# Kernel tuning notes

Hardware: AMD Instinct MI355X
Metric: run time of the kernel (lower is better)

## Reference

```python
import jax, jax.numpy as jnp
import numpy as np
import math

HIDDEN = 384
HEADS = 4
HEAD_DIM = HIDDEN // HEADS
B, T = 8, 2048


def _shift_rel(pos_tensor):
    # pos_tensor: [b, h, t, 2t-1] -> [b, h, t, t] (Transformer-XL shift trick)
    b, h, t, n = pos_tensor.shape
    zero_pad = jnp.zeros((b, h, t, 1), dtype=pos_tensor.dtype)
    padded = jnp.concatenate([zero_pad, pos_tensor], axis=-1)  # [b,h,t,n+1]
    padded = padded.reshape(b, h, n + 1, t)
    shifted = padded[:, :, 1:].reshape(b, h, t, n)
    return shifted[:, :, :, : n // 2 + 1]  # [b,h,t,t]


def setup_inputs() -> dict:
    key = jax.random.key(0)
    ks = jax.random.split(key, 12)
    s = 1.0 / math.sqrt(HIDDEN)
    inp = {
        "hidden_states": jax.random.normal(ks[0], (B, T, HIDDEN), jnp.float32),
        "pos_emb": jax.random.normal(ks[1], (1, 2 * T - 1, HIDDEN), jnp.float32),
        "attention_mask": jnp.ones((B, 1, T), jnp.int32),
        "Wq": jax.random.normal(ks[2], (HIDDEN, HIDDEN), jnp.float32) * s,
        "bq": jnp.zeros((HIDDEN,), jnp.float32),
        "Wk": jax.random.normal(ks[3], (HIDDEN, HIDDEN), jnp.float32) * s,
        "bk": jnp.zeros((HIDDEN,), jnp.float32),
        "Wv": jax.random.normal(ks[4], (HIDDEN, HIDDEN), jnp.float32) * s,
        "bv": jnp.zeros((HIDDEN,), jnp.float32),
        "Wo": jax.random.normal(ks[5], (HIDDEN, HIDDEN), jnp.float32) * s,
        "bo": jnp.zeros((HIDDEN,), jnp.float32),
        "Wpos": jax.random.normal(ks[6], (HIDDEN, HIDDEN), jnp.float32) * s,
        "pos_bias_u": jax.random.normal(ks[7], (HEADS, HEAD_DIM), jnp.float32) * s,
        "pos_bias_v": jax.random.normal(ks[8], (HEADS, HEAD_DIM), jnp.float32) * s,
    }
    return inp


def reference(hidden_states, pos_emb, attention_mask, Wq, bq, Wk, bk, Wv, bv,
              Wo, bo, Wpos, pos_bias_u, pos_bias_v):
    bsz, q_len, _ = hidden_states.shape
    # projections (nn.Linear applies x @ W.T + b; weights here stored as [in, out])
    q = (hidden_states @ Wq + bq).reshape(bsz, q_len, HEADS, HEAD_DIM)
    k = (hidden_states @ Wk + bk).reshape(bsz, q_len, HEADS, HEAD_DIM)
    v = (hidden_states @ Wv + bv).reshape(bsz, q_len, HEADS, HEAD_DIM)
    pos = (pos_emb @ Wpos).reshape(pos_emb.shape[0], -1, HEADS, HEAD_DIM)

    q_u = (q + pos_bias_u).transpose(0, 2, 1, 3)  # [b,h,t,d]
    q_v = (q + pos_bias_v).transpose(0, 2, 1, 3)

    # content score: [b,h,t,t]
    matrix_ac = jnp.einsum('bhqd,bkhd->bhqk', q_u, k)
    # position score: [b,h,t,2t-1] then shift
    matrix_bd = jnp.einsum('bhqd,pnhd->bhqn', q_v, pos)
    matrix_bd = _shift_rel(matrix_bd)

    scores = (matrix_ac + matrix_bd) / math.sqrt(HEAD_DIM)

    mask = (attention_mask[:, None] == 0)  # [b,1,1,t]
    min_val = jnp.finfo(scores.dtype).min
    scores = jnp.where(mask, min_val, scores)
    attn = jax.nn.softmax(scores, axis=-1)
    attn = jnp.where(mask, 0.0, attn)

    out = jnp.einsum('bhqk,bkhd->bqhd', attn, v).reshape(bsz, q_len, HIDDEN)
    return out @ Wo + bo
```

## Files before the change

### kernel.cpp

```cpp
#include <hip/hip_runtime.h>
#include <hip/hip_bf16.h>

#define TSEQ 2048
#define HID 384
#define NHEAD 4
#define HD 96
#define NBATCH 8

using bf16 = __bf16;
typedef bf16 bf16x8 __attribute__((ext_vector_type(8)));
typedef bf16 bf16x4 __attribute__((ext_vector_type(4)));
typedef float f32x4 __attribute__((ext_vector_type(4)));

static __device__ __forceinline__ f32x4 mfma16(bf16x8 a, bf16x8 b, f32x4 c) {
    return __builtin_amdgcn_mfma_f32_16x16x32_bf16(a, b, c, 0, 0, 0);
}

__global__ void k_conv8(const float* __restrict__ src, bf16* __restrict__ dst, int n8) {
    int t = blockIdx.x * 256 + threadIdx.x;
    if (t >= n8) return;
    const float4* s4 = reinterpret_cast<const float4*>(src);
    float4 a = s4[2 * t], b = s4[2 * t + 1];
    bf16x8 o;
    o[0] = (bf16)a.x; o[1] = (bf16)a.y; o[2] = (bf16)a.z; o[3] = (bf16)a.w;
    o[4] = (bf16)b.x; o[5] = (bf16)b.y; o[6] = (bf16)b.z; o[7] = (bf16)b.w;
    *reinterpret_cast<bf16x8*>(dst + 8 * t) = o;
}

__global__ void k_convT(const float* __restrict__ W, bf16* __restrict__ WT) {
    int t = blockIdx.x * 256 + threadIdx.x;
    int n = t / HID, k = t % HID;
    WT[t] = (bf16)W[(size_t)k * HID + n];
}

__launch_bounds__(256, 2)
__global__ void k_proj(const bf16* __restrict__ X, const bf16* __restrict__ P,
                       const bf16* __restrict__ wqT, const bf16* __restrict__ wkT,
                       const bf16* __restrict__ wvT, const bf16* __restrict__ wpT,
                       const float* __restrict__ bq, const float* __restrict__ bk,
                       const float* __restrict__ bv,
                       const float* __restrict__ pbu, const float* __restrict__ pbv,
                       bf16* __restrict__ qu, bf16* __restrict__ qv,
                       bf16* __restrict__ kws, bf16* __restrict__ vt,
                       bf16* __restrict__ pp) {
    __shared__ bf16 wt_lds[96][392];
    const float SC = 0.10206207262f;
    int mat = blockIdx.z;
    int m0 = blockIdx.x * 64;
    if (mat == 3 && m0 >= 4095) return;
    int n0 = blockIdx.y * 96;
    const bf16* A  = (mat == 3) ? P : X;
    const bf16* WT = (mat == 0) ? wqT : (mat == 1) ? wkT : (mat == 2) ? wvT : wpT;
    int tid = threadIdx.x;
    #pragma unroll
    for (int s = 0; s < 18; ++s) {
        int cc = tid + 256 * s;
        int r = cc / 48, ch = cc % 48;
        *reinterpret_cast<int4*>(&wt_lds[r][ch * 8]) =
            *reinterpret_cast<const int4*>(WT + (size_t)(n0 + r) * HID + ch * 8);
    }
    __syncthreads();
    int lane = tid & 63, w = tid >> 6;
    int c = lane & 15, g = lane >> 4;
    int arow = m0 + 16 * w + c;
    if (mat == 3 && arow > 4095) arow = 4095;
    const bf16* Abase = A + (size_t)arow * HID + 8 * g;
    f32x4 acc[6] = {};
    for (int ks = 0; ks < 12; ++ks) {
        bf16x8 a = *reinterpret_cast<const bf16x8*>(Abase + 32 * ks);
        #pragma unroll
        for (int jt = 0; jt < 6; ++jt) {
            bf16x8 b = *reinterpret_cast<const bf16x8*>(&wt_lds[16 * jt + c][32 * ks + 8 * g]);
            acc[jt] = mfma16(a, b, acc[jt]);
        }
    }
    int h = blockIdx.y;
    int rbase = m0 + 16 * w + 4 * g;
    if (mat == 0) {
        #pragma unroll
        for (int jt = 0; jt < 6; ++jt) {
            int n = n0 + 16 * jt + c;
            int d = 16 * jt + c;
            float bb = bq[n], bu = pbu[n], bvv = pbv[n];
            #pragma unroll
            for (int j = 0; j < 4; ++j) {
                int m = rbase + j;
                int b_ = m >> 11, t = m & 2047;
                size_t o = (((size_t)(b_ * NHEAD + h)) * TSEQ + t) * HD + d;
                float q = acc[jt][j] + bb;
                qu[o] = (bf16)((q + bu) * SC);
                qv[o] = (bf16)((q + bvv) * SC);
            }
        }
    } else if (mat == 1) {
        #pragma unroll
        for (int jt = 0; jt < 6; ++jt) {
            int n = n0 + 16 * jt + c;
            int d = 16 * jt + c;
            float bb = bk[n];
            #pragma unroll
            for (int j = 0; j < 4; ++j) {
                int m = rbase + j;
                int b_ = m >> 11, t = m & 2047;
                size_t o = (((size_t)(b_ * NHEAD + h)) * TSEQ + t) * HD + d;
                kws[o] = (bf16)(acc[jt][j] + bb);
            }
        }
    } else if (mat == 2) {
        #pragma unroll
        for (int jt = 0; jt < 6; ++jt) {
            int d = 16 * jt + c;
            float bb = bv[n0 + 16 * jt + c];
            int m = rbase;
            int b_ = m >> 11, t0 = m & 2047;
            size_t o = (((size_t)(b_ * NHEAD + h)) * HD + d) * TSEQ + t0;
            bf16x4 pk;
            #pragma unroll
            for (int j = 0; j < 4; ++j) pk[j] = (bf16)(acc[jt][j] + bb);
            *reinterpret_cast<bf16x4*>(vt + o) = pk;
        }
    } else {
        #pragma unroll
        for (int jt = 0; jt < 6; ++jt) {
            int d = 16 * jt + c;
            #pragma unroll
            for (int j = 0; j < 4; ++j) {
                int m = rbase + j;
                if (m < 4095) {
                    size_t o = ((size_t)h * 4096 + m) * HD + d;
                    pp[o] = (bf16)acc[jt][j];
                }
            }
        }
    }
}

__launch_bounds__(256, 2)
__global__ void k_attn(const bf16* __restrict__ qu, const bf16* __restrict__ qv,
                       const bf16* __restrict__ kws, const bf16* __restrict__ vt,
                       const bf16* __restrict__ pp, const int* __restrict__ mask,
                       bf16* __restrict__ out) {
    __shared__ bf16 k_lds[64][104];
    __shared__ bf16 pos_lds[128][104];
    __shared__ bf16 vt_lds[96][64];
    __shared__ bf16 win_lds[4][16][104];
    __shared__ bf16 p_lds[4][16][72];
    __shared__ float msk_lds[64];

    int bid = blockIdx.x;
    int v  = (bid & 7) * 128 + (bid >> 3);
    int qb = v & 31, bh = v >> 5;
    int q0 = qb * 64;
    int b_ = bh >> 2, h = bh & 3;

    int tid = threadIdx.x, lane = tid & 63, w = tid >> 6;
    int c = lane & 15, g = lane >> 4;
    const int n_base0 = TSEQ - 1 - 63 - q0;
    const float L2E = 1.44269504089f;
    int sw = 48 - 16 * w;

    int cc0 = tid, cc1 = tid + 256, cc2 = tid + 512;
    int kr0 = cc0 / 12, kc0 = cc0 % 12;
    int kr1 = cc1 / 12, kc1 = cc1 % 12;
    int kr2 = cc2 / 12, kc2 = cc2 % 12;
    int vr0 = cc0 >> 3, vc0 = cc0 & 7;
    int vr1 = cc1 >> 3, vc1 = cc1 & 7;
    int vr2 = cc2 >> 3, vc2 = cc2 & 7;
    int kO0 = kr0 * HD + kc0 * 8, kO1 = kr1 * HD + kc1 * 8, kO2 = kr2 * HD + kc2 * 8;
    int vO0 = vr0 * TSEQ + vc0 * 8, vO1 = vr1 * TSEQ + vc1 * 8, vO2 = vr2 * TSEQ + vc2 * 8;
    bf16* kP0 = &k_lds[kr0][kc0 * 8];
    bf16* kP1 = &k_lds[kr1][kc1 * 8];
    bf16* kP2 = &k_lds[kr2][kc2 * 8];
    bf16* vP0 = &vt_lds[vr0][(vc0 ^ (vr0 & 7)) * 8];
    bf16* vP1 = &vt_lds[vr1][(vc1 ^ (vr1 & 7)) * 8];
    bf16* vP2 = &vt_lds[vr2][(vc2 ^ (vr2 & 7)) * 8];
    int prow0 = n_base0 + 127 + kr0;
    int prow1 = n_base0 + 127 + kr1;
    int prow2 = n_base0 + 127 + kr2;
    int pO0 = prow0 * HD + kc0 * 8, pO1 = prow1 * HD + kc1 * 8, pO2 = prow2 * HD + kc2 * 8;
    bf16* pPA0 = &pos_lds[prow0 & 127][kc0 * 8];
    bf16* pPA1 = &pos_lds[prow1 & 127][kc1 * 8];
    bf16* pPA2 = &pos_lds[prow2 & 127][kc2 * 8];
    bf16* pPB0 = &pos_lds[(prow0 + 64) & 127][kc0 * 8];
    bf16* pPB1 = &pos_lds[(prow1 + 64) & 127][kc1 * 8];
    bf16* pPB2 = &pos_lds[(prow2 + 64) & 127][kc2 * 8];

    const bf16* kbP = kws + (size_t)bh * TSEQ * HD;
    const bf16* vbP = vt + (size_t)bh * HD * TSEQ;
    const bf16* pbP = pp + (size_t)h * 4096 * HD;
    const int*  mbP = mask + b_ * TSEQ;

    bf16x8 qu_f[3], qv_f[3];
    {
        size_t rowbase = ((size_t)bh * TSEQ + q0 + 16 * w + c) * HD + 8 * g;
        #pragma unroll
        for (int ds = 0; ds < 3; ++ds) {
            qu_f[ds] = *reinterpret_cast<const bf16x8*>(qu + rowbase + 32 * ds);
            qv_f[ds] = *reinterpret_cast<const bf16x8*>(qv + rowbase + 32 * ds);
        }
    }

    f32x4 acc_o[6] = {};
    float mrow = -3.0e38f, lrow = 0.f;

    {
        *reinterpret_cast<int4*>(kP0) = *reinterpret_cast<const int4*>(kbP + kO0);
        *reinterpret_cast<int4*>(kP1) = *reinterpret_cast<const int4*>(kbP + kO1);
        *reinterpret_cast<int4*>(kP2) = *reinterpret_cast<const int4*>(kbP + kO2);
        *reinterpret_cast<int4*>(vP0) = *reinterpret_cast<const int4*>(vbP + vO0);
        *reinterpret_cast<int4*>(vP1) = *reinterpret_cast<const int4*>(vbP + vO1);
        *reinterpret_cast<int4*>(vP2) = *reinterpret_cast<const int4*>(vbP + vO2);
        #pragma unroll
        for (int s = 0; s < 6; ++s) {
            int cc = tid + 256 * s; int r = cc / 12, ch = cc % 12;
            int n = n_base0 + r;
            *reinterpret_cast<int4*>(&pos_lds[n & 127][ch * 8]) =
                *reinterpret_cast<const int4*>(pbP + (size_t)n * HD + ch * 8);
        }
        if (tid < 64) msk_lds[tid] = (mbP[tid] == 0) ? -1e30f : 0.f;
    }
    __syncthreads();

    for (int kt = 0; kt < 32; ++kt) {
        int mclamp = (kt < 31) ? (kt + 1) * 64 : 31 * 64;
        const bf16* kb = kbP + (size_t)mclamp * HD;
        const bf16* vb = vbP + mclamp;
        const bf16* pb = pbP + (size_t)(64 * kt) * HD;
        int4 fK0 = *reinterpret_cast<const int4*>(kb + kO0);
        int4 fK1 = *reinterpret_cast<const int4*>(kb + kO1);
        int4 fK2 = *reinterpret_cast<const int4*>(kb + kO2);
        int4 fV0 = *reinterpret_cast<const int4*>(vb + vO0);
        int4 fV1 = *reinterpret_cast<const int4*>(vb + vO1);
        int4 fV2 = *reinterpret_cast<const int4*>(vb + vO2);
        int4 fP0 = *reinterpret_cast<const int4*>(pb + pO0);
        int4 fP1 = *reinterpret_cast<const int4*>(pb + pO1);
        int4 fP2 = *reinterpret_cast<const int4*>(pb + pO2);
        int  fM  = mbP[mclamp + lane];

        __builtin_amdgcn_s_setprio(1);
        f32x4 acc_s[4] = {};
        #pragma unroll
        for (int ds = 0; ds < 3; ++ds) {
            #pragma unroll
            for (int t = 0; t < 4; ++t) {
                bf16x8 a = *reinterpret_cast<const bf16x8*>(&k_lds[16 * t + c][32 * ds + 8 * g]);
                acc_s[t] = mfma16(a, qu_f[ds], acc_s[t]);
            }
        }
        f32x4 acc_w[5] = {};
        int wbase = n_base0 + 64 * kt + sw;
        #pragma unroll
        for (int ds = 0; ds < 3; ++ds) {
            #pragma unroll
            for (int t = 0; t < 5; ++t) {
                bf16x8 a = *reinterpret_cast<const bf16x8*>(
                    &pos_lds[(wbase + 16 * t + c) & 127][32 * ds + 8 * g]);
                acc_w[t] = mfma16(a, qv_f[ds], acc_w[t]);
            }
        }
        __builtin_amdgcn_s_setprio(0);
        #pragma unroll
        for (int t = 0; t < 5; ++t)
            #pragma unroll
            for (int j = 0; j < 4; ++j)
                win_lds[w][c][16 * t + 4 * g + j + c + 1] = (bf16)acc_w[t][j];
        __threadfence_block();

        float sA[4][4];
        #pragma unroll
        for (int t = 0; t < 4; ++t) {
            bf16x4 wv = *reinterpret_cast<const bf16x4*>(&win_lds[w][c][16 * t + 4 * g + 16]);
            float4 mv = *reinterpret_cast<const float4*>(&msk_lds[16 * t + 4 * g]);
            sA[t][0] = acc_s[t][0] + (float)wv[0] + mv.x;
            sA[t][1] = acc_s[t][1] + (float)wv[1] + mv.y;
            sA[t][2] = acc_s[t][2] + (float)wv[2] + mv.z;
            sA[t][3] = acc_s[t][3] + (float)wv[3] + mv.w;
        }
        float pm = sA[0][0];
        #pragma unroll
        for (int t = 0; t < 4; ++t)
            #pragma unroll
            for (int j = 0; j < 4; ++j) pm = fmaxf(pm, sA[t][j]);
        pm = fmaxf(pm, __shfl_xor(pm, 16));
        pm = fmaxf(pm, __shfl_xor(pm, 32));
        if (!__all(pm <= mrow + 8.0f)) {
            float mnew = fmaxf(mrow, pm);
            float alpha = exp2f((mrow - mnew) * L2E);
            mrow = mnew; lrow *= alpha;
            #pragma unroll
            for (int ot = 0; ot < 6; ++ot) acc_o[ot] *= alpha;
        }
        float rs = 0.f;
        #pragma unroll
        for (int t = 0; t < 4; ++t)
            #pragma unroll
            for (int j = 0; j < 4; ++j) {
                float p = exp2f((sA[t][j] - mrow) * L2E);
                sA[t][j] = p; rs += p;
            }
        rs += __shfl_xor(rs, 16);
        rs += __shfl_xor(rs, 32);
        lrow += rs;

        #pragma unroll
        for (int t = 0; t < 4; ++t) {
            bf16x4 pk;
            #pragma unroll
            for (int j = 0; j < 4; ++j) pk[j] = (bf16)sA[t][j];
            *reinterpret_cast<bf16x4*>(&p_lds[w][c][16 * t + 4 * g]) = pk;
        }
        __threadfence_block();
        __builtin_amdgcn_s_setprio(1);
        #pragma unroll
        for (int ds = 0; ds < 2; ++ds) {
            bf16x8 pb_ = *reinterpret_cast<const bf16x8*>(&p_lds[w][c][32 * ds + 8 * g]);
            #pragma unroll
            for (int ot = 0; ot < 6; ++ot) {
                int rr = 16 * ot + c;
                bf16x8 a = *reinterpret_cast<const bf16x8*>(
                    &vt_lds[rr][((4 * ds + g) ^ (rr & 7)) * 8]);
                acc_o[ot] = mfma16(a, pb_, acc_o[ot]);
            }
        }
        __builtin_amdgcn_s_setprio(0);

        __syncthreads();
        *reinterpret_cast<int4*>(kP0) = fK0;
        *reinterpret_cast<int4*>(kP1) = fK1;
        *reinterpret_cast<int4*>(kP2) = fK2;
        *reinterpret_cast<int4*>(vP0) = fV0;
        *reinterpret_cast<int4*>(vP1) = fV1;
        *reinterpret_cast<int4*>(vP2) = fV2;
        if (kt & 1) {
            *reinterpret_cast<int4*>(pPB0) = fP0;
            *reinterpret_cast<int4*>(pPB1) = fP1;
            *reinterpret_cast<int4*>(pPB2) = fP2;
        } else {
            *reinterpret_cast<int4*>(pPA0) = fP0;
            *reinterpret_cast<int4*>(pPA1) = fP1;
            *reinterpret_cast<int4*>(pPA2) = fP2;
        }
        if (tid < 64) msk_lds[tid] = (fM == 0) ? -1e30f : 0.f;
        __syncthreads();
    }

    float inv = 1.0f / lrow;
    size_t m = (size_t)b_ * TSEQ + q0 + 16 * w + c;
    bf16* ob = out + m * HID + h * HD + 4 * g;
    #pragma unroll
    for (int ot = 0; ot < 6; ++ot) {
        bf16x4 pk;
        #pragma unroll
        for (int j = 0; j < 4; ++j) pk[j] = (bf16)(acc_o[ot][j] * inv);
        *reinterpret_cast<bf16x4*>(&ob[16 * ot]) = pk;
    }
}

__launch_bounds__(256, 2)
__global__ void k_oproj(const bf16* __restrict__ A, const bf16* __restrict__ WT,
                        const float* __restrict__ bias, float* __restrict__ out) {
    __shared__ bf16 wt_lds[96][392];
    int m0 = blockIdx.x * 64, n0 = blockIdx.y * 96;
    int tid = threadIdx.x;
    #pragma unroll
    for (int s = 0; s < 18; ++s) {
        int cc = tid + 256 * s;
        int r = cc / 48, ch = cc % 48;
        *reinterpret_cast<int4*>(&wt_lds[r][ch * 8]) =
            *reinterpret_cast<const int4*>(WT + (size_t)(n0 + r) * HID + ch * 8);
    }
    __syncthreads();
    int lane = tid & 63, w = tid >> 6;
    int c = lane & 15, g = lane >> 4;
    const bf16* Abase = A + (size_t)(m0 + 16 * w + c) * HID + 8 * g;
    f32x4 acc[6] = {};
    for (int ks = 0; ks < 12; ++ks) {
        bf16x8 a = *reinterpret_cast<const bf16x8*>(Abase + 32 * ks);
        #pragma unroll
        for (int jt = 0; jt < 6; ++jt) {
            bf16x8 b = *reinterpret_cast<const bf16x8*>(&wt_lds[16 * jt + c][32 * ks + 8 * g]);
            acc[jt] = mfma16(a, b, acc[jt]);
        }
    }
    int rbase = m0 + 16 * w + 4 * g;
    #pragma unroll
    for (int jt = 0; jt < 6; ++jt) {
        int n = n0 + 16 * jt + c;
        float bb = bias[n];
        #pragma unroll
        for (int j = 0; j < 4; ++j)
            out[(size_t)(rbase + j) * HID + n] = acc[jt][j] + bb;
    }
}

extern "C" void kernel_launch(void* const* d_in, const int* in_sizes, int n_in,
                              void* d_out, int out_size, void* d_ws, size_t ws_size,
                              hipStream_t stream) {
    const float* hs  = (const float*)d_in[0];
    const float* pe  = (const float*)d_in[1];
    const int*   msk = (const int*)d_in[2];
    const float* Wq  = (const float*)d_in[3];
    const float* bq  = (const float*)d_in[4];
    const float* Wk  = (const float*)d_in[5];
    const float* bk  = (const float*)d_in[6];
    const float* Wv  = (const float*)d_in[7];
    const float* bv  = (const float*)d_in[8];
    const float* Wo  = (const float*)d_in[9];
    const float* bo  = (const float*)d_in[10];
    const float* Wp  = (const float*)d_in[11];
    const float* pbu = (const float*)d_in[12];
    const float* pbv = (const float*)d_in[13];

    char* ws = (char*)d_ws;
    size_t off = 0;
    auto alloc = [&](size_t b) { char* p = ws + off; off += (b + 255) & ~(size_t)255; return p; };
    bf16* Xb  = (bf16*)alloc((size_t)16384 * HID * 2);
    bf16* Pb  = (bf16*)alloc((size_t)4096 * HID * 2);
    bf16* wqT = (bf16*)alloc((size_t)HID * HID * 2);
    bf16* wkT = (bf16*)alloc((size_t)HID * HID * 2);
    bf16* wvT = (bf16*)alloc((size_t)HID * HID * 2);
    bf16* woT = (bf16*)alloc((size_t)HID * HID * 2);
    bf16* wpT = (bf16*)alloc((size_t)HID * HID * 2);
    bf16* qu  = (bf16*)alloc((size_t)NBATCH * NHEAD * TSEQ * HD * 2);
    bf16* qv  = (bf16*)alloc((size_t)NBATCH * NHEAD * TSEQ * HD * 2);
    bf16* kws = (bf16*)alloc((size_t)NBATCH * NHEAD * TSEQ * HD * 2);
    bf16* vt  = (bf16*)alloc((size_t)NBATCH * NHEAD * TSEQ * HD * 2);
    bf16* pp  = (bf16*)alloc((size_t)NHEAD * 4096 * HD * 2);
    bf16* ao  = (bf16*)alloc((size_t)16384 * HID * 2);

    k_conv8<<<3072, 256, 0, stream>>>(hs, Xb, 786432);
    k_conv8<<<768, 256, 0, stream>>>(pe, Pb, 196560);
    k_convT<<<576, 256, 0, stream>>>(Wq, wqT);
    k_convT<<<576, 256, 0, stream>>>(Wk, wkT);
    k_convT<<<576, 256, 0, stream>>>(Wv, wvT);
    k_convT<<<576, 256, 0, stream>>>(Wo, woT);
    k_convT<<<576, 256, 0, stream>>>(Wp, wpT);
    k_proj<<<dim3(256, 4, 4), 256, 0, stream>>>(Xb, Pb, wqT, wkT, wvT, wpT,
                                                bq, bk, bv, pbu, pbv,
                                                qu, qv, kws, vt, pp);
    k_attn<<<1024, 256, 0, stream>>>(qu, qv, kws, vt, pp, msk, ao);
    k_oproj<<<dim3(256, 4), 256, 0, stream>>>(ao, woT, bo, (float*)d_out);
}
```

Measured before the change: 291.4 us.

## Read positional rows from global memory to cut LDS and raise occupancy

Drops the 128-row positional LDS ring buffer and its staged prefetch. The position-score MFMAs now load their A-fragments straight from global memory, relying on cache reuse. The window and probability scratch buffers are merged into one LDS array with an extra fence, launch bounds go from 2 to 4 blocks per CU, and the block-to-(batch,head,qblock) mapping is reordered for L2 locality. The trade is uncoalesced-ish direct global loads on the critical path, which the added occupancy is meant to hide, and slight over-read padding is added to the pp allocation.

Result: slower. 400.1 us (+37.3%).

```diff
diff --git a/kernel.cpp b/kernel.cpp
--- a/kernel.cpp
+++ b/kernel.cpp
@@ -135,23 +135,23 @@
     }
 }
 
-__launch_bounds__(256, 2)
+__launch_bounds__(256, 4)
 __global__ void k_attn(const bf16* __restrict__ qu, const bf16* __restrict__ qv,
                        const bf16* __restrict__ kws, const bf16* __restrict__ vt,
                        const bf16* __restrict__ pp, const int* __restrict__ mask,
                        bf16* __restrict__ out) {
     __shared__ bf16 k_lds[64][104];
-    __shared__ bf16 pos_lds[128][104];
     __shared__ bf16 vt_lds[96][64];
-    __shared__ bf16 win_lds[4][16][104];
-    __shared__ bf16 p_lds[4][16][72];
+    __shared__ bf16 wp_lds[4][16][104];
     __shared__ float msk_lds[64];
 
     int bid = blockIdx.x;
-    int v  = (bid & 7) * 128 + (bid >> 3);
-    int qb = v & 31, bh = v >> 5;
+    int x = bid & 7, j5 = bid >> 3;
+    int h = x & 3;
+    int b_ = (x >> 2) * 4 + (j5 >> 5);
+    int qb = j5 & 31;
+    int bh = b_ * NHEAD + h;
     int q0 = qb * 64;
-    int b_ = bh >> 2, h = bh & 3;
 
     int tid = threadIdx.x, lane = tid & 63, w = tid >> 6;
     int c = lane & 15, g = lane >> 4;
@@ -174,16 +174,6 @@
     bf16* vP0 = &vt_lds[vr0][(vc0 ^ (vr0 & 7)) * 8];
     bf16* vP1 = &vt_lds[vr1][(vc1 ^ (vr1 & 7)) * 8];
     bf16* vP2 = &vt_lds[vr2][(vc2 ^ (vr2 & 7)) * 8];
-    int prow0 = n_base0 + 127 + kr0;
-    int prow1 = n_base0 + 127 + kr1;
-    int prow2 = n_base0 + 127 + kr2;
-    int pO0 = prow0 * HD + kc0 * 8, pO1 = prow1 * HD + kc1 * 8, pO2 = prow2 * HD + kc2 * 8;
-    bf16* pPA0 = &pos_lds[prow0 & 127][kc0 * 8];
-    bf16* pPA1 = &pos_lds[prow1 & 127][kc1 * 8];
-    bf16* pPA2 = &pos_lds[prow2 & 127][kc2 * 8];
-    bf16* pPB0 = &pos_lds[(prow0 + 64) & 127][kc0 * 8];
-    bf16* pPB1 = &pos_lds[(prow1 + 64) & 127][kc1 * 8];
-    bf16* pPB2 = &pos_lds[(prow2 + 64) & 127][kc2 * 8];
 
     const bf16* kbP = kws + (size_t)bh * TSEQ * HD;
     const bf16* vbP = vt + (size_t)bh * HD * TSEQ;
@@ -210,13 +200,6 @@
         *reinterpret_cast<int4*>(vP0) = *reinterpret_cast<const int4*>(vbP + vO0);
         *reinterpret_cast<int4*>(vP1) = *reinterpret_cast<const int4*>(vbP + vO1);
         *reinterpret_cast<int4*>(vP2) = *reinterpret_cast<const int4*>(vbP + vO2);
-        #pragma unroll
-        for (int s = 0; s < 6; ++s) {
-            int cc = tid + 256 * s; int r = cc / 12, ch = cc % 12;
-            int n = n_base0 + r;
-            *reinterpret_cast<int4*>(&pos_lds[n & 127][ch * 8]) =
-                *reinterpret_cast<const int4*>(pbP + (size_t)n * HD + ch * 8);
-        }
         if (tid < 64) msk_lds[tid] = (mbP[tid] == 0) ? -1e30f : 0.f;
     }
     __syncthreads();
@@ -225,18 +208,25 @@
         int mclamp = (kt < 31) ? (kt + 1) * 64 : 31 * 64;
         const bf16* kb = kbP + (size_t)mclamp * HD;
         const bf16* vb = vbP + mclamp;
-        const bf16* pb = pbP + (size_t)(64 * kt) * HD;
         int4 fK0 = *reinterpret_cast<const int4*>(kb + kO0);
         int4 fK1 = *reinterpret_cast<const int4*>(kb + kO1);
         int4 fK2 = *reinterpret_cast<const int4*>(kb + kO2);
         int4 fV0 = *reinterpret_cast<const int4*>(vb + vO0);
         int4 fV1 = *reinterpret_cast<const int4*>(vb + vO1);
         int4 fV2 = *reinterpret_cast<const int4*>(vb + vO2);
-        int4 fP0 = *reinterpret_cast<const int4*>(pb + pO0);
-        int4 fP1 = *reinterpret_cast<const int4*>(pb + pO1);
-        int4 fP2 = *reinterpret_cast<const int4*>(pb + pO2);
         int  fM  = mbP[mclamp + lane];
 
+        f32x4 acc_w[5] = {};
+        int wbase = n_base0 + 64 * kt + sw;
+        #pragma unroll
+        for (int t = 0; t < 5; ++t) {
+            const bf16* prow = pbP + (size_t)(wbase + 16 * t + c) * HD + 8 * g;
+            #pragma unroll
+            for (int ds = 0; ds < 3; ++ds) {
+                bf16x8 a = *reinterpret_cast<const bf16x8*>(prow + 32 * ds);
+                acc_w[t] = mfma16(a, qv_f[ds], acc_w[t]);
+            }
+        }
         __builtin_amdgcn_s_setprio(1);
         f32x4 acc_s[4] = {};
         #pragma unroll
@@ -247,29 +237,18 @@
                 acc_s[t] = mfma16(a, qu_f[ds], acc_s[t]);
             }
         }
-        f32x4 acc_w[5] = {};
-        int wbase = n_base0 + 64 * kt + sw;
-        #pragma unroll
-        for (int ds = 0; ds < 3; ++ds) {
-            #pragma unroll
-            for (int t = 0; t < 5; ++t) {
-                bf16x8 a = *reinterpret_cast<const bf16x8*>(
-                    &pos_lds[(wbase + 16 * t + c) & 127][32 * ds + 8 * g]);
-                acc_w[t] = mfma16(a, qv_f[ds], acc_w[t]);
-            }
-        }
         __builtin_amdgcn_s_setprio(0);
         #pragma unroll
         for (int t = 0; t < 5; ++t)
             #pragma unroll
             for (int j = 0; j < 4; ++j)
-                win_lds[w][c][16 * t + 4 * g + j + c + 1] = (bf16)acc_w[t][j];
+                wp_lds[w][c][16 * t + 4 * g + j + c + 1] = (bf16)acc_w[t][j];
         __threadfence_block();
 
         float sA[4][4];
         #pragma unroll
         for (int t = 0; t < 4; ++t) {
-            bf16x4 wv = *reinterpret_cast<const bf16x4*>(&win_lds[w][c][16 * t + 4 * g + 16]);
+            bf16x4 wv = *reinterpret_cast<const bf16x4*>(&wp_lds[w][c][16 * t + 4 * g + 16]);
             float4 mv = *reinterpret_cast<const float4*>(&msk_lds[16 * t + 4 * g]);
             sA[t][0] = acc_s[t][0] + (float)wv[0] + mv.x;
             sA[t][1] = acc_s[t][1] + (float)wv[1] + mv.y;
@@ -302,18 +281,19 @@
         rs += __shfl_xor(rs, 32);
         lrow += rs;
 
+        __threadfence_block();
         #pragma unroll
         for (int t = 0; t < 4; ++t) {
             bf16x4 pk;
             #pragma unroll
             for (int j = 0; j < 4; ++j) pk[j] = (bf16)sA[t][j];
-            *reinterpret_cast<bf16x4*>(&p_lds[w][c][16 * t + 4 * g]) = pk;
+            *reinterpret_cast<bf16x4*>(&wp_lds[w][c][16 * t + 4 * g]) = pk;
         }
         __threadfence_block();
         __builtin_amdgcn_s_setprio(1);
         #pragma unroll
         for (int ds = 0; ds < 2; ++ds) {
-            bf16x8 pb_ = *reinterpret_cast<const bf16x8*>(&p_lds[w][c][32 * ds + 8 * g]);
+            bf16x8 pb_ = *reinterpret_cast<const bf16x8*>(&wp_lds[w][c][32 * ds + 8 * g]);
             #pragma unroll
             for (int ot = 0; ot < 6; ++ot) {
                 int rr = 16 * ot + c;
@@ -331,15 +311,6 @@
         *reinterpret_cast<int4*>(vP0) = fV0;
         *reinterpret_cast<int4*>(vP1) = fV1;
         *reinterpret_cast<int4*>(vP2) = fV2;
-        if (kt & 1) {
-            *reinterpret_cast<int4*>(pPB0) = fP0;
-            *reinterpret_cast<int4*>(pPB1) = fP1;
-            *reinterpret_cast<int4*>(pPB2) = fP2;
-        } else {
-            *reinterpret_cast<int4*>(pPA0) = fP0;
-            *reinterpret_cast<int4*>(pPA1) = fP1;
-            *reinterpret_cast<int4*>(pPA2) = fP2;
-        }
         if (tid < 64) msk_lds[tid] = (fM == 0) ? -1e30f : 0.f;
         __syncthreads();
     }
@@ -425,7 +396,7 @@
     bf16* qv  = (bf16*)alloc((size_t)NBATCH * NHEAD * TSEQ * HD * 2);
     bf16* kws = (bf16*)alloc((size_t)NBATCH * NHEAD * TSEQ * HD * 2);
     bf16* vt  = (bf16*)alloc((size_t)NBATCH * NHEAD * TSEQ * HD * 2);
-    bf16* pp  = (bf16*)alloc((size_t)NHEAD * 4096 * HD * 2);
+    bf16* pp  = (bf16*)alloc((size_t)NHEAD * 4096 * HD * 2 + 4096);
     bf16* ao  = (bf16*)alloc((size_t)16384 * HID * 2);
 
     k_conv8<<<3072, 256, 0, stream>>>(hs, Xb, 786432);
```
